# Kernel tuning notes

Hardware: AMD Instinct MI355X
Metric: run time of the kernel (lower is better)

Reference implementation:

```python
import jax, jax.numpy as jnp
import numpy as np

N, E, D, H, C = 40000, 640000, 128, 4, 32  # nodes, edges, in_hid, heads, out_channels/head
NUM_NODE_TYPE, NUM_EDGE_TYPE = 8, 8
NEG_SLOPE = 0.2
EDGE_TYPE_SELF = 0


def setup_inputs() -> dict:
    key = jax.random.key(0)
    ks = jax.random.split(key, 12)
    x = jax.random.normal(ks[0], (N, D), dtype=jnp.float32)
    # build edges with no self-loops (the module filters src==dst before adding self-loops)
    src = jax.random.randint(ks[1], (E,), 0, N, dtype=jnp.int32)
    off = jax.random.randint(ks[2], (E,), 1, N, dtype=jnp.int32)
    dst = (src + off) % N
    edge_index = jnp.stack([src, dst])  # [2, E]
    node_type = jax.random.randint(ks[3], (N,), 0, NUM_NODE_TYPE, dtype=jnp.int32)
    edge_type = jax.random.randint(ks[4], (E,), 0, NUM_EDGE_TYPE, dtype=jnp.int32)
    g = 0.05
    Wq = jax.random.normal(ks[5], (H * C, D), dtype=jnp.float32) * g
    Wk = jax.random.normal(ks[6], (H * C, D), dtype=jnp.float32) * g
    Wv = jax.random.normal(ks[7], (H * C, D), dtype=jnp.float32) * g
    att_i = jax.random.normal(ks[8], (1, H, C), dtype=jnp.float32) * g
    att_j = jax.random.normal(ks[9], (1, H, C), dtype=jnp.float32) * g
    bias = jnp.zeros((H * C,), dtype=jnp.float32)
    node_emb_table = jax.random.normal(ks[10], (NUM_NODE_TYPE, D), dtype=jnp.float32) * g
    edge_emb_table = jax.random.normal(ks[11], (NUM_EDGE_TYPE, D), dtype=jnp.float32) * g
    return {"x": x, "edge_index": edge_index, "node_type": node_type,
            "edge_type": edge_type, "Wq": Wq, "Wk": Wk, "Wv": Wv,
            "att_i": att_i, "att_j": att_j, "bias": bias,
            "node_emb_table": node_emb_table, "edge_emb_table": edge_emb_table}


def reference(x, edge_index, node_type, edge_type, Wq, Wk, Wv,
              att_i, att_j, bias, node_emb_table, edge_emb_table):
    n = x.shape[0]
    # node-type embedding add
    x = x + node_emb_table[node_type]                       # [N, D]
    xq = x @ Wq.T                                           # [N, H*C]
    # add self-loops (input edges contain no src==dst by construction)
    self_idx = jnp.arange(n, dtype=edge_index.dtype)
    src = jnp.concatenate([edge_index[0], self_idx])        # [E+N]
    dst = jnp.concatenate([edge_index[1], self_idx])        # [E+N]
    et = jnp.concatenate([edge_type,
                          jnp.full((n,), EDGE_TYPE_SELF, dtype=edge_type.dtype)])
    edge_emb = edge_emb_table[et]                           # [E+N, D]
    # message: per-edge gather + K/V linear + additive attention
    x_j = x[src] + edge_emb                                 # [E+N, D]
    xq_i = xq[dst].reshape(-1, H, C)                        # [E+N, H, C]
    x_k = (x_j @ Wk.T).reshape(-1, H, C)
    x_v = (x_j @ Wv.T).reshape(-1, H, C)
    alpha = (xq_i * att_i).sum(-1) + (x_k * att_j).sum(-1)  # [E+N, H]
    alpha = jax.nn.leaky_relu(alpha, NEG_SLOPE)
    # segment softmax over destination nodes (PyG softmax, eps=1e-16)
    amax = jax.ops.segment_max(alpha, dst, num_segments=n)  # [N, H]
    alpha = jnp.exp(alpha - amax[dst])
    denom = jax.ops.segment_sum(alpha, dst, num_segments=n)
    alpha = alpha / (denom[dst] + 1e-16)
    # scatter-add weighted values
    out = jax.ops.segment_sum(x_v * alpha[..., None], dst, num_segments=n)  # [N, H, C]
    return out.reshape(n, H * C) + bias
```

## Files before the change

kernel.cpp:

```cpp
#include <hip/hip_runtime.h>
#include <math.h>

#define NN 40000
#define NE 640000
#define D 128
#define NH 4
#define NC 32
#define NEG 0.2f

#define NBKT 625
#define NBIN 500
#define SEGC 16

typedef __attribute__((ext_vector_type(8))) short bf16x8;
typedef __attribute__((ext_vector_type(4))) float f32x4;

__device__ __forceinline__ unsigned pack_bf16(float a, float b) {
  unsigned ua = __float_as_uint(a), ub = __float_as_uint(b);
  ua = (ua + 0x7FFFu + ((ua >> 16) & 1u)) >> 16;
  ub = (ub + 0x7FFFu + ((ub >> 16) & 1u)) & 0xFFFF0000u;
  return ub | ua;
}

__device__ __forceinline__ bf16x8 to_bf16x8(float4 a, float4 b) {
  union { bf16x8 v; unsigned u[4]; } r;
  r.u[0] = pack_bf16(a.x, a.y);
  r.u[1] = pack_bf16(a.z, a.w);
  r.u[2] = pack_bf16(b.x, b.y);
  r.u[3] = pack_bf16(b.z, b.w);
  return r.v;
}

__device__ __forceinline__ float4 f4add(float4 a, float4 b) {
  return make_float4(a.x + b.x, a.y + b.y, a.z + b.z, a.w + b.w);
}

__global__ __launch_bounds__(256) void k_pb(
    const int* __restrict__ ei, const int* __restrict__ etype,
    unsigned* __restrict__ binbuf,
    const float* __restrict__ Wq, const float* __restrict__ Wk,
    const float* __restrict__ Wv,
    const float* __restrict__ att_i, const float* __restrict__ att_j,
    const float* __restrict__ eemb,
    float* __restrict__ ev, float* __restrict__ a_et,
    unsigned* __restrict__ Wvh) {
  __shared__ unsigned smem[10640];
  int b = blockIdx.x, t = threadIdx.x;

  if (b < NBIN) {
    unsigned* lbuf = smem;
    int* hist = (int*)(smem + 10000);
    for (int j = t; j < NBKT; j += 256) hist[j] = 0;
    __syncthreads();
    int e0 = b * 1280;
#pragma unroll
    for (int k = 0; k < 5; ++k) {
      int e = e0 + k * 256 + t;
      int src = ei[e];
      int dst = ei[NE + e];
      int et  = etype[e];
      int bk = dst >> 6;
      int r = atomicAdd(&hist[bk], 1);
      if (r < SEGC)
        lbuf[bk * SEGC + r] =
            (unsigned)src | ((unsigned)et << 16) | ((unsigned)(dst & 63) << 19);
    }
    __syncthreads();
    for (int j = t; j < NBKT; j += 256) {
      unsigned c = (unsigned)min(hist[j], SEGC);
      unsigned s0 = (c == 0) ? 0u : (lbuf[j * SEGC] & 0x01FFFFFFu);
      lbuf[j * SEGC] = s0 | (c << 27);
    }
    __syncthreads();
    for (int j = t; j < NBKT; j += 256) {
      const uint4* __restrict__ s4 = (const uint4*)(lbuf + j * SEGC);
      uint4* __restrict__ d4 = (uint4*)(binbuf + ((size_t)j * NBIN + b) * SEGC);
      d4[0] = s4[0]; d4[1] = s4[1]; d4[2] = s4[2]; d4[3] = s4[3];
    }
    return;
  }

  float* sm = (float*)smem;
  int tb = b - NBIN;
  if (tb == 0) {
    for (int j = t; j < 1024; j += 256) {
      int isq = (j < 512);
      int h = (j >> 7) & 3, d = j & 127;
      const float* __restrict__ Wm = isq ? Wq : Wk;
      const float* __restrict__ am = isq ? att_i : att_j;
      float s = 0.f;
#pragma unroll
      for (int c = 0; c < NC; ++c) s = fmaf(am[h * NC + c], Wm[(h * NC + c) * D + d], s);
      sm[j] = s;
    }
    __syncthreads();
    for (int j = t; j < 1024; j += 256) {
      int r = j >> 6;
      int c2 = (j & 63) * 2;
      float a = 0.f, bb = 0.f;
      if (r < 8) { a = sm[r * 128 + c2]; bb = sm[r * 128 + c2 + 1]; }
      Wvh[(128 + r) * 64 + (j & 63)] = pack_bf16(a, bb);
    }
    if (t < 32) {
      int ty = t >> 2, hh = t & 3;
      const float* wrow = sm + 512 + hh * 128;
      const float* __restrict__ emb = eemb + ty * D;
      float s = 0.f;
#pragma unroll 8
      for (int d = 0; d < D; ++d) s = fmaf(wrow[d], emb[d], s);
      a_et[t] = s;
    }
  } else if (tb <= 8) {
    int ty = tb - 1;
    if (t < 128) sm[t] = eemb[ty * D + t];
    __syncthreads();
    if (t < 128) {
      const float4* __restrict__ wr = (const float4*)(Wv + (size_t)t * D);
      const float4* __restrict__ er = (const float4*)sm;
      float s = 0.f;
#pragma unroll
      for (int k = 0; k < 32; ++k) {
        float4 ww = wr[k], ee = er[k];
        s = fmaf(ww.x, ee.x, s); s = fmaf(ww.y, ee.y, s);
        s = fmaf(ww.z, ee.z, s); s = fmaf(ww.w, ee.w, s);
      }
      ev[ty * D + t] = s;
    }
  } else {
    int j0 = (tb - 9) * 1024;
    for (int j = j0 + t; j < j0 + 1024; j += 256)
      Wvh[j] = pack_bf16(Wv[2 * j], Wv[2 * j + 1]);
  }
}

__global__ __launch_bounds__(256) void k_xv(
    const float* __restrict__ x, const int* __restrict__ node_type,
    const float* __restrict__ nemb, const unsigned* __restrict__ Wvh,
    unsigned* __restrict__ xvh, float* __restrict__ aq, float* __restrict__ ak) {
  int bb = blockIdx.x, t = threadIdx.x;
  int w = t >> 6, l = t & 63;
  int quad = l >> 4, col = l & 15;
  int n0w = bb * 64 + w * 16;
  int node = n0w + col;
  int ntA = node_type[node];
  const float4* __restrict__ xr = (const float4*)(x + (size_t)node * D);
  const float4* __restrict__ nr = (const float4*)(nemb + (size_t)ntA * D);
  bf16x8 afr[4];
#pragma unroll
  for (int s = 0; s < 4; ++s) {
    const float4* p = xr + s * 8 + quad * 2;
    const float4* q4 = nr + s * 8 + quad * 2;
    afr[s] = to_bf16x8(f4add(p[0], q4[0]), f4add(p[1], q4[1]));
  }
  f32x4 acc[9];
#pragma unroll
  for (int ct = 0; ct < 9; ++ct) acc[ct] = (f32x4){0.f, 0.f, 0.f, 0.f};
#pragma unroll
  for (int ct = 0; ct < 9; ++ct) {
    const unsigned* __restrict__ brow = Wvh + (size_t)(ct * 16 + col) * 64;
#pragma unroll
    for (int s = 0; s < 4; ++s) {
      bf16x8 bfr = *(const bf16x8*)(brow + s * 16 + quad * 4);
      acc[ct] = __builtin_amdgcn_mfma_f32_16x16x32_bf16(afr[s], bfr, acc[ct], 0, 0, 0);
    }
  }
  int nodes[4];
#pragma unroll
  for (int r = 0; r < 4; ++r) nodes[r] = n0w + quad * 4 + r;
#pragma unroll
  for (int ct = 0; ct < 8; ++ct) {
#pragma unroll
    for (int r = 0; r < 4; ++r) {
      float val = acc[ct][r];
      float pv = __shfl_xor(val, 1);
      if (!(col & 1)) {
        xvh[nodes[r] * 64 + ct * 8 + (col >> 1)] = pack_bf16(val, pv);
      }
    }
  }
  if (col < 4) {
#pragma unroll
    for (int r = 0; r < 4; ++r) aq[nodes[r] * NH + col] = acc[8][r];
  } else if (col < 8) {
#pragma unroll
    for (int r = 0; r < 4; ++r) ak[nodes[r] * NH + (col - 4)] = acc[8][r];
  }
}

__global__ __launch_bounds__(512) void k_gb(
    const unsigned* __restrict__ binbuf,
    const float* __restrict__ aq, const float* __restrict__ ak,
    const float* __restrict__ a_et, const unsigned* __restrict__ xvh,
    const float* __restrict__ ev, const float* __restrict__ bias,
    float* __restrict__ out) {
  __shared__ int lcnt[64];
  __shared__ unsigned csr[4096];
  int b = blockIdx.x, t = threadIdx.x;
  if (t < 64) lcnt[t] = 0;
  __syncthreads();
  if (t < NBIN) {
    const unsigned* __restrict__ sp = binbuf + ((size_t)b * NBIN + t) * SEGC;
    uint4 a0 = *(const uint4*)sp;
    uint4 a1 = *(const uint4*)(sp + 4);
    uint4 a2 = *(const uint4*)(sp + 8);
    uint4 a3 = *(const uint4*)(sp + 12);
    unsigned rr[16] = {a0.x, a0.y, a0.z, a0.w, a1.x, a1.y, a1.z, a1.w,
                       a2.x, a2.y, a2.z, a2.w, a3.x, a3.y, a3.z, a3.w};
    int cnt = (int)(rr[0] >> 27);
    rr[0] &= 0x01FFFFFFu;
#pragma unroll
    for (int j = 0; j < SEGC; ++j) {
      if (j < cnt) {
        unsigned rec = rr[j];
        int loc = (int)(rec >> 19) & 63;
        int r = atomicAdd(&lcnt[loc], 1);
        if (r < 63) csr[(loc << 6) + r] = rec & 0x7FFFFu;
      }
    }
  }
  __syncthreads();
  int w = t >> 6, l = t & 63;
  int g = l >> 3, q = l & 7;
  int h = q >> 1;
  const uint4* __restrict__ xv4 = (const uint4*)xvh;
  const float4* __restrict__ ep = (const float4*)(ev + g * D + 16 * q);
  float4 ea0 = ep[0], ea1 = ep[1], ea2 = ep[2], ea3 = ep[3];
#pragma unroll 1
  for (int j4 = 0; j4 < 8; ++j4) {
    int loc = (w << 3) + j4;
    int n = (b << 6) + loc;
    float aqh = aq[n * NH + h];
    int deg = min(lcnt[loc], 63);
    int m = deg + 1;
    float acc[16];
#pragma unroll
    for (int k = 0; k < 16; ++k) acc[k] = 0.f;
    float ps[8];
#pragma unroll
    for (int k = 0; k < 8; ++k) ps[k] = 0.f;
    int iters = (m + 7) >> 3;
    int i = g;
    bool val = (i < m);
    unsigned rec = (val && i < deg) ? csr[(loc << 6) + i] : (unsigned)n;
    int src = (int)(rec & 0xFFFFu), etc = (int)(rec >> 16);
    float sA = ak[src * NH + h] + a_et[etc * NH + h];
    uint4 vb0 = xv4[src * 16 + 2 * q];
    uint4 vb1 = xv4[src * 16 + 2 * q + 1];
    for (int it = 0; it < iters; ++it) {
      int i2 = i + 8;
      bool v2 = (i2 < m);
      float sAn = 0.f; int etn = 0;
      uint4 vb0n = make_uint4(0, 0, 0, 0), vb1n = make_uint4(0, 0, 0, 0);
      if (it + 1 < iters) {
        unsigned rec2 = (v2 && i2 < deg) ? csr[(loc << 6) + i2] : (unsigned)n;
        int s2 = (int)(rec2 & 0xFFFFu);
        etn = (int)(rec2 >> 16);
        sAn = ak[s2 * NH + h] + a_et[etn * NH + h];
        vb0n = xv4[s2 * 16 + 2 * q];
        vb1n = xv4[s2 * 16 + 2 * q + 1];
      }
      float s = aqh + sA;
      s = (s > 0.f) ? s : NEG * s;
      float p = val ? __expf(s) : 0.f;
#pragma unroll
      for (int tt = 0; tt < 8; ++tt) ps[tt] += (etc == tt) ? p : 0.f;
      float f[16];
      f[0]  = __uint_as_float(vb0.x << 16); f[1]  = __uint_as_float(vb0.x & 0xFFFF0000u);
      f[2]  = __uint_as_float(vb0.y << 16); f[3]  = __uint_as_float(vb0.y & 0xFFFF0000u);
      f[4]  = __uint_as_float(vb0.z << 16); f[5]  = __uint_as_float(vb0.z & 0xFFFF0000u);
      f[6]  = __uint_as_float(vb0.w << 16); f[7]  = __uint_as_float(vb0.w & 0xFFFF0000u);
      f[8]  = __uint_as_float(vb1.x << 16); f[9]  = __uint_as_float(vb1.x & 0xFFFF0000u);
      f[10] = __uint_as_float(vb1.y << 16); f[11] = __uint_as_float(vb1.y & 0xFFFF0000u);
      f[12] = __uint_as_float(vb1.z << 16); f[13] = __uint_as_float(vb1.z & 0xFFFF0000u);
      f[14] = __uint_as_float(vb1.w << 16); f[15] = __uint_as_float(vb1.w & 0xFFFF0000u);
#pragma unroll
      for (int k = 0; k < 16; ++k) acc[k] = fmaf(p, f[k], acc[k]);
      i = i2; val = v2; sA = sAn; etc = etn; vb0 = vb0n; vb1 = vb1n;
    }
#pragma unroll
    for (int tt = 0; tt < 8; ++tt) {
      ps[tt] += __shfl_xor(ps[tt], 8);
      ps[tt] += __shfl_xor(ps[tt], 16);
      ps[tt] += __shfl_xor(ps[tt], 32);
    }
    float dsum = ((ps[0] + ps[1]) + (ps[2] + ps[3])) + ((ps[4] + ps[5]) + (ps[6] + ps[7]));
    float psg = ps[0];
#pragma unroll
    for (int tt = 1; tt < 8; ++tt) psg = (g == tt) ? ps[tt] : psg;
    acc[0]  = fmaf(psg, ea0.x, acc[0]);
    acc[1]  = fmaf(psg, ea0.y, acc[1]);
    acc[2]  = fmaf(psg, ea0.z, acc[2]);
    acc[3]  = fmaf(psg, ea0.w, acc[3]);
    acc[4]  = fmaf(psg, ea1.x, acc[4]);
    acc[5]  = fmaf(psg, ea1.y, acc[5]);
    acc[6]  = fmaf(psg, ea1.z, acc[6]);
    acc[7]  = fmaf(psg, ea1.w, acc[7]);
    acc[8]  = fmaf(psg, ea2.x, acc[8]);
    acc[9]  = fmaf(psg, ea2.y, acc[9]);
    acc[10] = fmaf(psg, ea2.z, acc[10]);
    acc[11] = fmaf(psg, ea2.w, acc[11]);
    acc[12] = fmaf(psg, ea3.x, acc[12]);
    acc[13] = fmaf(psg, ea3.y, acc[13]);
    acc[14] = fmaf(psg, ea3.z, acc[14]);
    acc[15] = fmaf(psg, ea3.w, acc[15]);
#pragma unroll
    for (int k = 0; k < 16; ++k) {
      acc[k] += __shfl_xor(acc[k], 8);
      acc[k] += __shfl_xor(acc[k], 16);
      acc[k] += __shfl_xor(acc[k], 32);
    }
    if (g == 0) {
      float inv = 1.f / (dsum + 1e-16f);
      const float4* __restrict__ b4 = (const float4*)(bias + 16 * q);
      float4* __restrict__ op = (float4*)(out + (size_t)n * D + 16 * q);
#pragma unroll
      for (int k4 = 0; k4 < 4; ++k4) {
        float4 bb = b4[k4];
        op[k4] = make_float4(acc[4 * k4 + 0] * inv + bb.x,
                             acc[4 * k4 + 1] * inv + bb.y,
                             acc[4 * k4 + 2] * inv + bb.z,
                             acc[4 * k4 + 3] * inv + bb.w);
      }
    }
  }
}

extern "C" void kernel_launch(void* const* d_in, const int* in_sizes, int n_in,
                              void* d_out, int out_size, void* d_ws, size_t ws_size,
                              hipStream_t stream) {
  const float* x      = (const float*)d_in[0];
  const int*   ei     = (const int*)d_in[1];
  const int*   ntype  = (const int*)d_in[2];
  const int*   etype  = (const int*)d_in[3];
  const float* Wq     = (const float*)d_in[4];
  const float* Wk     = (const float*)d_in[5];
  const float* Wv     = (const float*)d_in[6];
  const float* att_i  = (const float*)d_in[7];
  const float* att_j  = (const float*)d_in[8];
  const float* bias   = (const float*)d_in[9];
  const float* nemb   = (const float*)d_in[10];
  const float* eemb   = (const float*)d_in[11];
  float* out = (float*)d_out;

  float* ws     = (float*)d_ws;
  unsigned* xvh = (unsigned*)ws;
  float* aq     = ws + (size_t)NN * 64;
  float* ak     = aq + NN * NH;
  float* ev     = ak + NN * NH;
  float* a_et   = ev + 1024;
  unsigned* Wvh = (unsigned*)(a_et + 32);
  unsigned* binbuf = (unsigned*)(Wvh + 9216);

  k_pb<<<dim3(NBIN + 17), dim3(256), 0, stream>>>(ei, etype, binbuf,
                                                  Wq, Wk, Wv, att_i, att_j, eemb,
                                                  ev, a_et, Wvh);
  k_xv<<<dim3(625), dim3(256), 0, stream>>>(x, ntype, nemb, Wvh, xvh, aq, ak);
  k_gb<<<dim3(NBKT), dim3(512), 0, stream>>>(binbuf, aq, ak, a_et,
                                             xvh, ev, bias, out);
}
```

Measured before the change: 176.8 us.

## Split gather kernel by head halves, doubling blocks and edge-level parallelism

The gather/softmax kernel now launches two blocks per 64-node bucket, each handling half of the 128 output channels (two heads). Within a wave, 16 edge lanes with 4 channel lanes replace 8 edge lanes with 8 channel lanes, which halves the per-node iteration count and adds one shuffle reduction step. This is meant to raise parallelism and latency hiding for the gather-bound loop. In exchange, each block rebuilds the shared CSR bucket (duplicate bin reads and atomics), and there is extra shuffle work.

```diff
diff --git a/kernel.cpp b/kernel.cpp
--- a/kernel.cpp
+++ b/kernel.cpp
@@ -195,7 +195,11 @@
     float* __restrict__ out) {
   __shared__ int lcnt[64];
   __shared__ unsigned csr[4096];
-  int b = blockIdx.x, t = threadIdx.x;
+  int bid = blockIdx.x, t = threadIdx.x;
+  int xx = bid & 7;
+  int half = xx >> 2;
+  int b = (bid >> 3) * 4 + (xx & 3);
+  if (b >= NBKT) return;
   if (t < 64) lcnt[t] = 0;
   __syncthreads();
   if (t < NBIN) {
@@ -220,11 +224,13 @@
   }
   __syncthreads();
   int w = t >> 6, l = t & 63;
-  int g = l >> 3, q = l & 7;
-  int h = q >> 1;
+  int gp = l >> 2, qp = l & 3;
+  int h = 2 * half + (qp >> 1);
+  int gt = gp & 7;
   const uint4* __restrict__ xv4 = (const uint4*)xvh;
-  const float4* __restrict__ ep = (const float4*)(ev + g * D + 16 * q);
+  const float4* __restrict__ ep = (const float4*)(ev + gt * D + 64 * half + 16 * qp);
   float4 ea0 = ep[0], ea1 = ep[1], ea2 = ep[2], ea3 = ep[3];
+  int cbase = half * 8 + 2 * qp;
 #pragma unroll 1
   for (int j4 = 0; j4 < 8; ++j4) {
     int loc = (w << 3) + j4;
@@ -238,16 +244,16 @@
     float ps[8];
 #pragma unroll
     for (int k = 0; k < 8; ++k) ps[k] = 0.f;
-    int iters = (m + 7) >> 3;
-    int i = g;
+    int iters = (m + 15) >> 4;
+    int i = gp;
     bool val = (i < m);
     unsigned rec = (val && i < deg) ? csr[(loc << 6) + i] : (unsigned)n;
     int src = (int)(rec & 0xFFFFu), etc = (int)(rec >> 16);
     float sA = ak[src * NH + h] + a_et[etc * NH + h];
-    uint4 vb0 = xv4[src * 16 + 2 * q];
-    uint4 vb1 = xv4[src * 16 + 2 * q + 1];
+    uint4 vb0 = xv4[src * 16 + cbase];
+    uint4 vb1 = xv4[src * 16 + cbase + 1];
     for (int it = 0; it < iters; ++it) {
-      int i2 = i + 8;
+      int i2 = i + 16;
       bool v2 = (i2 < m);
       float sAn = 0.f; int etn = 0;
       uint4 vb0n = make_uint4(0, 0, 0, 0), vb1n = make_uint4(0, 0, 0, 0);
@@ -256,8 +262,8 @@
         int s2 = (int)(rec2 & 0xFFFFu);
         etn = (int)(rec2 >> 16);
         sAn = ak[s2 * NH + h] + a_et[etn * NH + h];
-        vb0n = xv4[s2 * 16 + 2 * q];
-        vb1n = xv4[s2 * 16 + 2 * q + 1];
+        vb0n = xv4[s2 * 16 + cbase];
+        vb1n = xv4[s2 * 16 + cbase + 1];
       }
       float s = aqh + sA;
       s = (s > 0.f) ? s : NEG * s;
@@ -279,6 +285,7 @@
     }
 #pragma unroll
     for (int tt = 0; tt < 8; ++tt) {
+      ps[tt] += __shfl_xor(ps[tt], 4);
       ps[tt] += __shfl_xor(ps[tt], 8);
       ps[tt] += __shfl_xor(ps[tt], 16);
       ps[tt] += __shfl_xor(ps[tt], 32);
@@ -286,7 +293,8 @@
     float dsum = ((ps[0] + ps[1]) + (ps[2] + ps[3])) + ((ps[4] + ps[5]) + (ps[6] + ps[7]));
     float psg = ps[0];
 #pragma unroll
-    for (int tt = 1; tt < 8; ++tt) psg = (g == tt) ? ps[tt] : psg;
+    for (int tt = 1; tt < 8; ++tt) psg = (gt == tt) ? ps[tt] : psg;
+    psg = (gp < 8) ? psg : 0.f;
     acc[0]  = fmaf(psg, ea0.x, acc[0]);
     acc[1]  = fmaf(psg, ea0.y, acc[1]);
     acc[2]  = fmaf(psg, ea0.z, acc[2]);
@@ -305,14 +313,15 @@
     acc[15] = fmaf(psg, ea3.w, acc[15]);
 #pragma unroll
     for (int k = 0; k < 16; ++k) {
+      acc[k] += __shfl_xor(acc[k], 4);
       acc[k] += __shfl_xor(acc[k], 8);
       acc[k] += __shfl_xor(acc[k], 16);
       acc[k] += __shfl_xor(acc[k], 32);
     }
-    if (g == 0) {
+    if (gp == 0) {
       float inv = 1.f / (dsum + 1e-16f);
-      const float4* __restrict__ b4 = (const float4*)(bias + 16 * q);
-      float4* __restrict__ op = (float4*)(out + (size_t)n * D + 16 * q);
+      const float4* __restrict__ b4 = (const float4*)(bias + 64 * half + 16 * qp);
+      float4* __restrict__ op = (float4*)(out + (size_t)n * D + 64 * half + 16 * qp);
 #pragma unroll
       for (int k4 = 0; k4 < 4; ++k4) {
         float4 bb = b4[k4];
@@ -355,6 +364,6 @@
                                                   Wq, Wk, Wv, att_i, att_j, eemb,
                                                   ev, a_et, Wvh);
   k_xv<<<dim3(625), dim3(256), 0, stream>>>(x, ntype, nemb, Wvh, xvh, aq, ak);
-  k_gb<<<dim3(NBKT), dim3(512), 0, stream>>>(binbuf, aq, ak, a_et,
-                                             xvh, ev, bias, out);
-}
+  k_gb<<<dim3(157 * 8), dim3(512), 0, stream>>>(binbuf, aq, ak, a_et,
+                                                xvh, ev, bias, out);
+}
```

Result: slower. 213.6 us (+20.8%).
